# Performance work log

Measured on AMD Instinct MI355X. Metric: run time of the kernel, lower is better.

Reference implementation:

```python
import math
import jax, jax.numpy as jnp
import numpy as np

SCALE = math.sqrt(128.0)  # NOTE: original code MULTIPLIES by sqrt(128)
DROPOUT_P = 0.1


def setup_inputs() -> dict:
    key = jax.random.key(0)
    kq, kk, kv = jax.random.split(key, 3)
    B, Q, V, H = 4, 4096, 4096, 128
    return {
        "query": jax.random.normal(kq, (B, Q, H), dtype=jnp.float32),
        "key": jax.random.normal(kk, (B, V, H), dtype=jnp.float32),
        "value": jax.random.normal(kv, (B, V, H), dtype=jnp.float32),
    }


def reference(query, key, value):
    # qk: [B, Q, V]
    qk = jnp.einsum("bqh,bvh->bqv", query, key)
    scaled_qk = qk * SCALE
    softmax_qk = jax.nn.softmax(scaled_qk, axis=-1)
    # inverted dropout with a fixed RNG key (deterministic reference)
    dk = jax.random.key(42)
    keep = jax.random.bernoulli(dk, 1.0 - DROPOUT_P, softmax_qk.shape)
    dropout_qk = jnp.where(keep, softmax_qk / (1.0 - DROPOUT_P), 0.0)
    # output: [B, Q, H]
    return jnp.einsum("bqv,bvh->bqh", dropout_qk, value)
```

## Files before the change

### kernel.cpp

```cpp
#include <hip/hip_runtime.h>
#include <stdint.h>

#define NBATCH 4
#define NQ 4096
#define NV 4096
#define HD 128

#define SCL2E ((float)(11.31370849898476 * 1.4426950408889634))

#define KEEP_THRESH 3865470464u
#define EPS_SKIP 1e-6f

#define TILE_USH 24576
#define WS_NEEDED ((size_t)NBATCH * 64 * TILE_USH * 2)

#define PSTR 72
#define VLSTR 142

#define KSTR 144
#define VSTR 76

typedef __attribute__((ext_vector_type(8))) short short8;
typedef __attribute__((ext_vector_type(4))) float floatx4;
typedef unsigned int uint;
typedef unsigned short ushort;

__device__ __forceinline__ ushort bf16rne(float f) {
    uint u = __float_as_uint(f);
    u = (u + 0x7fffu + ((u >> 16) & 1u)) >> 16;
    return (ushort)u;
}
__device__ __forceinline__ float bf2f(ushort h) {
    return __uint_as_float(((uint)h) << 16);
}

template <int CTRL>
__device__ __forceinline__ float dppmov(float x) {
    return __int_as_float(__builtin_amdgcn_update_dpp(
        0, __float_as_int(x), CTRL, 0xF, 0xF, true));
}
__device__ __forceinline__ float row_max16(float x) {
    x = fmaxf(x, dppmov<0xB1>(x));
    x = fmaxf(x, dppmov<0x4E>(x));
    x = fmaxf(x, dppmov<0x141>(x));
    x = fmaxf(x, dppmov<0x140>(x));
    return x;
}
__device__ __forceinline__ float row_sum16(float x) {
    x += dppmov<0xB1>(x);
    x += dppmov<0x4E>(x);
    x += dppmov<0x141>(x);
    x += dppmov<0x140>(x);
    return x;
}

__device__ __forceinline__ uint rotl(uint x, int r) { return (x << r) | (x >> (32 - r)); }

__device__ __forceinline__ uint threefry_bits(uint j) {
    uint x0 = 0u;
    uint x1 = j;
    const uint k0 = 0u, k1 = 42u, k2 = 0u ^ 42u ^ 0x1BD11BDAu;
    x0 += k0; x1 += k1;
#define TFR4(a,b,c,d) \
    x0 += x1; x1 = rotl(x1, a); x1 ^= x0; \
    x0 += x1; x1 = rotl(x1, b); x1 ^= x0; \
    x0 += x1; x1 = rotl(x1, c); x1 ^= x0; \
    x0 += x1; x1 = rotl(x1, d); x1 ^= x0;
    TFR4(13, 15, 26, 6)
    x0 += k1; x1 += k2 + 1u;
    TFR4(17, 29, 16, 24)
    x0 += k2; x1 += k0 + 2u;
    TFR4(13, 15, 26, 6)
    x0 += k0; x1 += k1 + 3u;
    TFR4(17, 29, 16, 24)
    x0 += k1; x1 += k2 + 4u;
    TFR4(13, 15, 26, 6)
    x0 += k2; x1 += k0 + 5u;
#undef TFR4
    return x0 ^ x1;
}

__global__ __launch_bounds__(256)
void prepass(const float* __restrict__ Kg, const float* __restrict__ Vg,
             ushort* __restrict__ W) {
    __shared__ ushort vls[64 * VLSTR];
    const int rec  = blockIdx.x >> 1;
    const int half = blockIdx.x & 1;
    const int bb = rec >> 6;
    const int t  = rec & 63;
    const int v0 = t * 64;
    const size_t kvbase = (size_t)bb * NV * HD;
    ushort* dst = W + ((size_t)bb * 64 + t) * TILE_USH;
    const int tid = threadIdx.x;

    if (half == 0) {
        ushort* dkh = dst;
        ushort* dkl = dst + 8192;
#pragma unroll
        for (int i = 0; i < 4; ++i) {
            int lc = i * 256 + tid;
            int v = lc >> 4, c = lc & 15;
            const float* src = Kg + kvbase + (size_t)(v0 + v) * HD + c * 8;
            float x[8];
            *(float4*)&x[0] = *(const float4*)src;
            *(float4*)&x[4] = *(const float4*)(src + 4);
            uint H[4], L[4];
#pragma unroll
            for (int k = 0; k < 4; ++k) {
                ushort h0 = bf16rne(x[2 * k]),     h1 = bf16rne(x[2 * k + 1]);
                ushort l0 = bf16rne(x[2 * k] - bf2f(h0));
                ushort l1 = bf16rne(x[2 * k + 1] - bf2f(h1));
                H[k] = (uint)h0 | ((uint)h1 << 16);
                L[k] = (uint)l0 | ((uint)l1 << 16);
            }
            int pos = (((c >> 2) * 4 + (v >> 4)) * 64 + (c & 3) * 16 + (v & 15)) * 8;
            *(uint4*)&dkh[pos] = *(uint4*)H;
            *(uint4*)&dkl[pos] = *(uint4*)L;
        }
    } else {
        ushort* dvt = dst + 16384;
#pragma unroll
        for (int i = 0; i < 8; ++i) {
            int idx = i * 256 + tid;
            int v = idx >> 5, hq = idx & 31;
            float4 a = *(const float4*)(Vg + kvbase + (size_t)(v0 + v) * HD + hq * 4);
            uint w0 = (uint)bf16rne(a.x) | ((uint)bf16rne(a.y) << 16);
            uint w1 = (uint)bf16rne(a.z) | ((uint)bf16rne(a.w) << 16);
            *(uint*)&vls[v * VLSTR + hq * 4]     = w0;
            *(uint*)&vls[v * VLSTR + hq * 4 + 2] = w1;
        }
        __syncthreads();
#pragma unroll
        for (int i = 0; i < 4; ++i) {
            int lc = i * 256 + tid;
            int h = lc >> 3, c2 = lc & 7;
            uint Wd[4];
#pragma unroll
            for (int m = 0; m < 8; m += 2) {
                ushort a  = vls[(c2 * 8 + m) * VLSTR + h];
                ushort b2 = vls[(c2 * 8 + m + 1) * VLSTR + h];
                Wd[m >> 1] = (uint)a | ((uint)b2 << 16);
            }
            int pos = (((c2 >> 2) * 8 + (h >> 4)) * 64 + (c2 & 3) * 16 + (h & 15)) * 8;
            *(uint4*)&dvt[pos] = *(uint4*)Wd;
        }
    }
}

__global__ __launch_bounds__(256, 2)
void fa_mfma7(const float* __restrict__ Qg, const ushort* __restrict__ Wk,
              float* __restrict__ Og) {
    __shared__ ushort pls[4][32 * PSTR];
    __shared__ float obuf[3][32 * 128];
    __shared__ float mlbuf[3][32][2];

    const int tid  = threadIdx.x;
    const int wave = tid >> 6;
    const int lane = tid & 63;
    const int r    = lane & 15;
    const int qd   = lane >> 4;
    const int blockRow0 = blockIdx.x * 32;
    const int b = blockRow0 >> 12;
    const ushort* kvw = Wk + (size_t)b * 64 * TILE_USH;

    short8 qfh[2][4], qfl[2][4];
#pragma unroll
    for (int mr = 0; mr < 2; ++mr) {
        const float* qp = Qg + (size_t)(blockRow0 + mr * 16 + r) * HD + qd * 8;
#pragma unroll
        for (int kc = 0; kc < 4; ++kc) {
            float x[8];
            *(float4*)&x[0] = *(const float4*)(qp + kc * 32);
            *(float4*)&x[4] = *(const float4*)(qp + kc * 32 + 4);
#pragma unroll
            for (int j = 0; j < 8; ++j) {
                ushort h = bf16rne(x[j]);
                qfh[mr][kc][j] = (short)h;
                qfl[mr][kc][j] = (short)bf16rne(x[j] - bf2f(h));
            }
        }
    }

    floatx4 oacc[2][8];
#pragma unroll
    for (int mr = 0; mr < 2; ++mr)
#pragma unroll
        for (int n = 0; n < 8; ++n) oacc[mr][n] = (floatx4){0.f, 0.f, 0.f, 0.f};
    float m2[2][4], lr[2][4];
#pragma unroll
    for (int mr = 0; mr < 2; ++mr)
#pragma unroll
        for (int g = 0; g < 4; ++g) { m2[mr][g] = -INFINITY; lr[mr][g] = 0.f; }

    for (int t = wave; t < 64; t += 4) {
        const ushort* tK = kvw + (size_t)t * TILE_USH;
        const ushort* tV = tK + 16384;
        const int v0 = t * 64;

        floatx4 cf[2][4];
#pragma unroll
        for (int mr = 0; mr < 2; ++mr)
#pragma unroll
            for (int nb = 0; nb < 4; ++nb) cf[mr][nb] = (floatx4){0.f, 0.f, 0.f, 0.f};
#pragma unroll
        for (int kc = 0; kc < 4; ++kc) {
            short8 kh[4], kl[4];
#pragma unroll
            for (int nb = 0; nb < 4; ++nb) {
                int off = ((kc * 4 + nb) * 64 + lane) * 8;
                kh[nb] = *(const short8*)&tK[off];
                kl[nb] = *(const short8*)&tK[8192 + off];
            }
#pragma unroll
            for (int nb = 0; nb < 4; ++nb)
#pragma unroll
                for (int mr = 0; mr < 2; ++mr) {
                    cf[mr][nb] = __builtin_amdgcn_mfma_f32_16x16x32_bf16(qfh[mr][kc], kh[nb], cf[mr][nb], 0, 0, 0);
                    cf[mr][nb] = __builtin_amdgcn_mfma_f32_16x16x32_bf16(qfh[mr][kc], kl[nb], cf[mr][nb], 0, 0, 0);
                    cf[mr][nb] = __builtin_amdgcn_mfma_f32_16x16x32_bf16(qfl[mr][kc], kh[nb], cf[mr][nb], 0, 0, 0);
                }
        }

        bool act[2];
#pragma unroll
        for (int mr = 0; mr < 2; ++mr) {
            float ts[4][4], p[4][4], alpha[4], lnew[4], tsum[4];
#pragma unroll
            for (int nb = 0; nb < 4; ++nb)
#pragma unroll
                for (int g = 0; g < 4; ++g) ts[nb][g] = cf[mr][nb][g] * SCL2E;
#pragma unroll
            for (int g = 0; g < 4; ++g) {
                float tmx = fmaxf(fmaxf(ts[0][g], ts[1][g]), fmaxf(ts[2][g], ts[3][g]));
                tmx = row_max16(tmx);
                float mn = fmaxf(m2[mr][g], tmx);
                alpha[g] = __builtin_amdgcn_exp2f(m2[mr][g] - mn);
                m2[mr][g] = mn;
            }
#pragma unroll
            for (int g = 0; g < 4; ++g) {
                float s = 0.f;
#pragma unroll
                for (int nb = 0; nb < 4; ++nb) {
                    p[nb][g] = __builtin_amdgcn_exp2f(ts[nb][g] - m2[mr][g]);
                    s += p[nb][g];
                }
                s = row_sum16(s);
                tsum[g] = s;
                lnew[g] = lr[mr][g] * alpha[g] + s;
                lr[mr][g] = lnew[g];
            }
            bool rowneed = false;
#pragma unroll
            for (int g = 0; g < 4; ++g) rowneed |= (tsum[g] > EPS_SKIP * lnew[g]);
            act[mr] = __any(rowneed);

            if (act[mr]) {
#pragma unroll
                for (int n = 0; n < 8; ++n)
#pragma unroll
                    for (int g = 0; g < 4; ++g) oacc[mr][n][g] *= alpha[g];
#pragma unroll
                for (int nb = 0; nb < 4; ++nb) {
#pragma unroll
                    for (int g = 0; g < 4; ++g) {
                        if (__any(p[nb][g] > EPS_SKIP * lnew[g])) {
                            uint j = (uint)(blockRow0 + mr * 16 + qd * 4 + g) * (uint)NV
                                   + (uint)(v0 + nb * 16 + r);
                            if (threefry_bits(j) >= KEEP_THRESH) p[nb][g] = 0.f;
                        }
                        pls[wave][(mr * 16 + qd * 4 + g) * PSTR + nb * 16 + r] =
                            (ushort)(__float_as_uint(p[nb][g]) >> 16);
                    }
                }
            }
        }

        if (act[0] | act[1]) {
            __asm__ volatile("s_waitcnt lgkmcnt(0)" ::: "memory");
#pragma unroll
            for (int mr = 0; mr < 2; ++mr) {
                if (!act[mr]) continue;
#pragma unroll
                for (int kc2 = 0; kc2 < 2; ++kc2) {
                    short8 pa = *(const short8*)&pls[wave][(mr * 16 + r) * PSTR + kc2 * 32 + qd * 8];
#pragma unroll
                    for (int n = 0; n < 8; ++n) {
                        short8 vb = *(const short8*)&tV[((kc2 * 8 + n) * 64 + lane) * 8];
                        oacc[mr][n] = __builtin_amdgcn_mfma_f32_16x16x32_bf16(pa, vb, oacc[mr][n], 0, 0, 0);
                    }
                }
            }
        }
    }

    if (wave >= 1) {
#pragma unroll
        for (int mr = 0; mr < 2; ++mr) {
            if (r == 0) {
#pragma unroll
                for (int g = 0; g < 4; ++g) {
                    mlbuf[wave - 1][mr * 16 + qd * 4 + g][0] = m2[mr][g];
                    mlbuf[wave - 1][mr * 16 + qd * 4 + g][1] = lr[mr][g];
                }
            }
#pragma unroll
            for (int n = 0; n < 8; ++n)
#pragma unroll
                for (int g = 0; g < 4; ++g)
                    obuf[wave - 1][(mr * 16 + qd * 4 + g) * 128 + n * 16 + r] = oacc[mr][n][g];
        }
    }
    __syncthreads();
    if (wave == 0) {
#pragma unroll
        for (int mr = 0; mr < 2; ++mr) {
            float a0[4], aw[3][4], inv[4];
#pragma unroll
            for (int g = 0; g < 4; ++g) {
                int row = mr * 16 + qd * 4 + g;
                float mn = m2[mr][g];
#pragma unroll
                for (int i = 0; i < 3; ++i) mn = fmaxf(mn, mlbuf[i][row][0]);
                a0[g] = __builtin_amdgcn_exp2f(m2[mr][g] - mn);
                float l = lr[mr][g] * a0[g];
#pragma unroll
                for (int i = 0; i < 3; ++i) {
                    aw[i][g] = __builtin_amdgcn_exp2f(mlbuf[i][row][0] - mn);
                    l += mlbuf[i][row][1] * aw[i][g];
                }
                inv[g] = 1.0f / (0.9f * l);
            }
#pragma unroll
            for (int n = 0; n < 8; ++n)
#pragma unroll
                for (int g = 0; g < 4; ++g) {
                    int row = mr * 16 + qd * 4 + g;
                    float o = oacc[mr][n][g] * a0[g];
#pragma unroll
                    for (int i = 0; i < 3; ++i)
                        o += obuf[i][row * 128 + n * 16 + r] * aw[i][g];
                    Og[(size_t)(blockRow0 + row) * HD + n * 16 + r] = o * inv[g];
                }
        }
    }
}

__global__ __launch_bounds__(256)
void fa_mfma(const float* __restrict__ Qg, const float* __restrict__ Kg,
             const float* __restrict__ Vg, float* __restrict__ Og) {
    __shared__ ushort khi[64 * KSTR];
    __shared__ ushort klo[64 * KSTR];
    __shared__ ushort vt[128 * VSTR];
    __shared__ ushort plsf[4][16 * PSTR];

    const int tid  = threadIdx.x;
    const int wave = tid >> 6;
    const int lane = tid & 63;
    const int r    = lane & 15;
    const int qd   = lane >> 4;
    const int blockRow0 = blockIdx.x * 64;
    const int b = blockRow0 >> 12;
    const int waveRow0 = blockRow0 + wave * 16;
    const size_t kvbase = (size_t)b * NV * HD;

    short8 qfh[4], qfl[4];
    {
        const float* qp = Qg + (size_t)(waveRow0 + r) * HD + qd * 8;
#pragma unroll
        for (int kc = 0; kc < 4; ++kc) {
            float x[8];
            *(float4*)&x[0] = *(const float4*)(qp + kc * 32);
            *(float4*)&x[4] = *(const float4*)(qp + kc * 32 + 4);
#pragma unroll
            for (int j = 0; j < 8; ++j) {
                ushort h = bf16rne(x[j]);
                qfh[kc][j] = (short)h;
                qfl[kc][j] = (short)bf16rne(x[j] - bf2f(h));
            }
        }
    }

    floatx4 oacc[8];
#pragma unroll
    for (int n = 0; n < 8; ++n) oacc[n] = (floatx4){0.f, 0.f, 0.f, 0.f};
    float m2[4] = {-INFINITY, -INFINITY, -INFINITY, -INFINITY};
    float lr[4] = {0.f, 0.f, 0.f, 0.f};

    for (int v0 = 0; v0 < NV; v0 += 64) {
        __syncthreads();
#pragma unroll
        for (int i = 0; i < 8; ++i) {
            int f = i * 256 + tid;
            int v = f >> 5;
            int h = (f & 31) * 4;
            float4 kv = *(const float4*)(Kg + kvbase + (size_t)(v0 + v) * HD + h);
            ushort4 hh, ll;
            hh.x = bf16rne(kv.x); ll.x = bf16rne(kv.x - bf2f(hh.x));
            hh.y = bf16rne(kv.y); ll.y = bf16rne(kv.y - bf2f(hh.y));
            hh.z = bf16rne(kv.z); ll.z = bf16rne(kv.z - bf2f(hh.z));
            hh.w = bf16rne(kv.w); ll.w = bf16rne(kv.w - bf2f(hh.w));
            *(ushort4*)&khi[v * KSTR + h] = hh;
            *(ushort4*)&klo[v * KSTR + h] = ll;
        }
        {
            int hp = tid & 63, rp = tid >> 6;
            int h = hp * 2;
            const float* vpb = Vg + kvbase + (size_t)v0 * HD + h;
#pragma unroll
            for (int i = 0; i < 8; ++i) {
                int v = i * 8 + rp * 2;
                float2 a = *(const float2*)(vpb + (size_t)v * HD);
                float2 c = *(const float2*)(vpb + (size_t)(v + 1) * HD);
                uint w0 = (uint)bf16rne(a.x) | ((uint)bf16rne(c.x) << 16);
                uint w1 = (uint)bf16rne(a.y) | ((uint)bf16rne(c.y) << 16);
                *(uint*)&vt[h * VSTR + v]       = w0;
                *(uint*)&vt[(h + 1) * VSTR + v] = w1;
            }
        }
        __syncthreads();

        floatx4 cf[4];
#pragma unroll
        for (int nb = 0; nb < 4; ++nb) cf[nb] = (floatx4){0.f, 0.f, 0.f, 0.f};
#pragma unroll
        for (int kc = 0; kc < 4; ++kc) {
#pragma unroll
            for (int nb = 0; nb < 4; ++nb) {
                int off = (nb * 16 + r) * KSTR + kc * 32 + qd * 8;
                short8 kh = *(const short8*)&khi[off];
                short8 kl = *(const short8*)&klo[off];
                cf[nb] = __builtin_amdgcn_mfma_f32_16x16x32_bf16(qfh[kc], kh, cf[nb], 0, 0, 0);
                cf[nb] = __builtin_amdgcn_mfma_f32_16x16x32_bf16(qfh[kc], kl, cf[nb], 0, 0, 0);
                cf[nb] = __builtin_amdgcn_mfma_f32_16x16x32_bf16(qfl[kc], kh, cf[nb], 0, 0, 0);
            }
        }

        float ts[4][4], p[4][4];
#pragma unroll
        for (int nb = 0; nb < 4; ++nb)
#pragma unroll
            for (int g = 0; g < 4; ++g) ts[nb][g] = cf[nb][g] * SCL2E;

        float tsum[4], alpha[4], lnew[4];
#pragma unroll
        for (int g = 0; g < 4; ++g) {
            float tmx = fmaxf(fmaxf(ts[0][g], ts[1][g]), fmaxf(ts[2][g], ts[3][g]));
#pragma unroll
            for (int off = 1; off < 16; off <<= 1)
                tmx = fmaxf(tmx, __shfl_xor(tmx, off));
            float mn = fmaxf(m2[g], tmx);
            alpha[g] = __builtin_amdgcn_exp2f(m2[g] - mn);
            m2[g] = mn;
        }
#pragma unroll
        for (int g = 0; g < 4; ++g) {
            float s = 0.f;
#pragma unroll
            for (int nb = 0; nb < 4; ++nb) {
                p[nb][g] = __builtin_amdgcn_exp2f(ts[nb][g] - m2[g]);
                s += p[nb][g];
            }
#pragma unroll
            for (int off = 1; off < 16; off <<= 1)
                s += __shfl_xor(s, off);
            tsum[g] = s;
            lnew[g] = lr[g] * alpha[g] + s;
            lr[g] = lnew[g];
        }

        bool rowneed = false;
#pragma unroll
        for (int g = 0; g < 4; ++g) rowneed |= (tsum[g] > 1e-8f * lnew[g]);

        if (__any(rowneed)) {
#pragma unroll
            for (int n = 0; n < 8; ++n)
#pragma unroll
                for (int g = 0; g < 4; ++g) oacc[n][g] *= alpha[g];

#pragma unroll
            for (int nb = 0; nb < 4; ++nb) {
                bool nbneed = false;
#pragma unroll
                for (int g = 0; g < 4; ++g) nbneed |= (p[nb][g] > 1e-8f * lnew[g]);
                if (__any(nbneed)) {
#pragma unroll
                    for (int g = 0; g < 4; ++g) {
                        uint j = (uint)(waveRow0 + qd * 4 + g) * (uint)NV
                               + (uint)(v0 + nb * 16 + r);
                        if (threefry_bits(j) >= KEEP_THRESH) p[nb][g] = 0.f;
                    }
                }
#pragma unroll
                for (int g = 0; g < 4; ++g)
                    plsf[wave][(qd * 4 + g) * PSTR + nb * 16 + r] = bf16rne(p[nb][g]);
            }
            __asm__ volatile("s_waitcnt lgkmcnt(0)" ::: "memory");

#pragma unroll
            for (int kc2 = 0; kc2 < 2; ++kc2) {
                short8 pa = *(const short8*)&plsf[wave][r * PSTR + kc2 * 32 + qd * 8];
#pragma unroll
                for (int n = 0; n < 8; ++n) {
                    int off = (n * 16 + r) * VSTR + kc2 * 32 + qd * 8;
                    ushort4 u0 = *(const ushort4*)&vt[off];
                    ushort4 u1 = *(const ushort4*)&vt[off + 4];
                    short8 vb;
                    vb[0] = (short)u0.x; vb[1] = (short)u0.y; vb[2] = (short)u0.z; vb[3] = (short)u0.w;
                    vb[4] = (short)u1.x; vb[5] = (short)u1.y; vb[6] = (short)u1.z; vb[7] = (short)u1.w;
                    oacc[n] = __builtin_amdgcn_mfma_f32_16x16x32_bf16(pa, vb, oacc[n], 0, 0, 0);
                }
            }
        }
    }

    float inv[4];
#pragma unroll
    for (int g = 0; g < 4; ++g) inv[g] = 1.0f / (0.9f * lr[g]);
#pragma unroll
    for (int n = 0; n < 8; ++n)
#pragma unroll
        for (int g = 0; g < 4; ++g)
            Og[(size_t)(waveRow0 + qd * 4 + g) * HD + n * 16 + r] = oacc[n][g] * inv[g];
}

extern "C" void kernel_launch(void* const* d_in, const int* in_sizes, int n_in,
                              void* d_out, int out_size, void* d_ws, size_t ws_size,
                              hipStream_t stream) {
    (void)in_sizes; (void)n_in; (void)out_size;
    const float* Qg = (const float*)d_in[0];
    const float* Kg = (const float*)d_in[1];
    const float* Vg = (const float*)d_in[2];
    float* Og = (float*)d_out;
    if (ws_size >= WS_NEEDED) {
        ushort* W = (ushort*)d_ws;
        prepass<<<dim3(512), 256, 0, stream>>>(Kg, Vg, W);
        fa_mfma7<<<dim3(NBATCH * NQ / 32), 256, 0, stream>>>(Qg, (const ushort*)W, Og);
    } else {
        fa_mfma<<<dim3(NBATCH * NQ / 64), 256, 0, stream>>>(Qg, Kg, Vg, Og);
    }
}
```

Before: 199.0 us.

## Split KV tiles across eight waves with shared running max and tree merge

Doubles the block to 512 threads so eight waves each take every eighth KV tile, and merges partial softmax states with a log-depth tree reduction through shared memory. Tiles are skipped using a block-shared per-row running max with a fixed log2 margin, replacing the relative-sum epsilon test. The scale is folded into Q before the bf16 split, and the accumulator rescale is skipped when the max does not grow. The goal is more parallelism per row block and less exp, rescale and dropout-hash work on tiles that contribute nothing. The cost is more barriers and lower register budget per thread, and the margin-based skip is an approximation that differs from the old epsilon criterion.

```diff
diff --git a/kernel.cpp b/kernel.cpp
--- a/kernel.cpp
+++ b/kernel.cpp
@@ -9,7 +9,9 @@
 #define SCL2E ((float)(11.31370849898476 * 1.4426950408889634))
 
 #define KEEP_THRESH 3865470464u
-#define EPS_SKIP 1e-6f
+
+#define SKIP_MARGIN 27.0f
+#define DROP_MARGIN 20.0f
 
 #define TILE_USH 24576
 #define WS_NEEDED ((size_t)NBATCH * 64 * TILE_USH * 2)
@@ -147,12 +149,12 @@
     }
 }
 
-__global__ __launch_bounds__(256, 2)
+__global__ __launch_bounds__(512, 4)
 void fa_mfma7(const float* __restrict__ Qg, const ushort* __restrict__ Wk,
               float* __restrict__ Og) {
-    __shared__ ushort pls[4][32 * PSTR];
-    __shared__ float obuf[3][32 * 128];
-    __shared__ float mlbuf[3][32][2];
+    __shared__ __align__(16) float smemf[16384];
+    __shared__ float mlbuf[4][32][2];
+    __shared__ float gmx[32];
 
     const int tid  = threadIdx.x;
     const int wave = tid >> 6;
@@ -162,6 +164,9 @@
     const int blockRow0 = blockIdx.x * 32;
     const int b = blockRow0 >> 12;
     const ushort* kvw = Wk + (size_t)b * 64 * TILE_USH;
+    ushort* pls = (ushort*)smemf + wave * (32 * PSTR);
+
+    if (tid < 32) gmx[tid] = -1e30f;
 
     short8 qfh[2][4], qfl[2][4];
 #pragma unroll
@@ -174,9 +179,10 @@
             *(float4*)&x[4] = *(const float4*)(qp + kc * 32 + 4);
 #pragma unroll
             for (int j = 0; j < 8; ++j) {
-                ushort h = bf16rne(x[j]);
+                float xs = x[j] * SCL2E;
+                ushort h = bf16rne(xs);
                 qfh[mr][kc][j] = (short)h;
-                qfl[mr][kc][j] = (short)bf16rne(x[j] - bf2f(h));
+                qfl[mr][kc][j] = (short)bf16rne(xs - bf2f(h));
             }
         }
     }
@@ -190,9 +196,11 @@
 #pragma unroll
     for (int mr = 0; mr < 2; ++mr)
 #pragma unroll
-        for (int g = 0; g < 4; ++g) { m2[mr][g] = -INFINITY; lr[mr][g] = 0.f; }
-
-    for (int t = wave; t < 64; t += 4) {
+        for (int g = 0; g < 4; ++g) { m2[mr][g] = -1e30f; lr[mr][g] = 0.f; }
+
+    __syncthreads();
+
+    for (int t = wave; t < 64; t += 8) {
         const ushort* tK = kvw + (size_t)t * TILE_USH;
         const ushort* tV = tK + 16384;
         const int v0 = t * 64;
@@ -224,54 +232,70 @@
         bool act[2];
 #pragma unroll
         for (int mr = 0; mr < 2; ++mr) {
-            float ts[4][4], p[4][4], alpha[4], lnew[4], tsum[4];
-#pragma unroll
-            for (int nb = 0; nb < 4; ++nb)
-#pragma unroll
-                for (int g = 0; g < 4; ++g) ts[nb][g] = cf[mr][nb][g] * SCL2E;
+            float tmx[4], gm[4];
 #pragma unroll
             for (int g = 0; g < 4; ++g) {
-                float tmx = fmaxf(fmaxf(ts[0][g], ts[1][g]), fmaxf(ts[2][g], ts[3][g]));
-                tmx = row_max16(tmx);
-                float mn = fmaxf(m2[mr][g], tmx);
-                alpha[g] = __builtin_amdgcn_exp2f(m2[mr][g] - mn);
-                m2[mr][g] = mn;
-            }
+                float v = fmaxf(fmaxf(cf[mr][0][g], cf[mr][1][g]),
+                                fmaxf(cf[mr][2][g], cf[mr][3][g]));
+                tmx[g] = row_max16(v);
+            }
+            bool rowact = false;
+#pragma unroll
+            for (int g = 0; g < 4; ++g) {
+                gm[g] = gmx[mr * 16 + qd * 4 + g];
+                rowact |= (tmx[g] > fmaxf(m2[mr][g], gm[g]) - SKIP_MARGIN);
+            }
+#pragma unroll
+            for (int g = 0; g < 4; ++g)
+                if (r == 0 && tmx[g] > gm[g]) gmx[mr * 16 + qd * 4 + g] = tmx[g];
+            act[mr] = __any(rowact);
+            if (!act[mr]) continue;
+
+            float alpha[4];
+            bool nm = false;
+#pragma unroll
+            for (int g = 0; g < 4; ++g) nm |= (tmx[g] > m2[mr][g]);
+            if (__any(nm)) {
+#pragma unroll
+                for (int g = 0; g < 4; ++g) {
+                    float mn = fmaxf(m2[mr][g], tmx[g]);
+                    alpha[g] = __builtin_amdgcn_exp2f(m2[mr][g] - mn);
+                    m2[mr][g] = mn;
+                }
+#pragma unroll
+                for (int n = 0; n < 8; ++n)
+#pragma unroll
+                    for (int g = 0; g < 4; ++g) oacc[mr][n][g] *= alpha[g];
+            } else {
+#pragma unroll
+                for (int g = 0; g < 4; ++g) alpha[g] = 1.f;
+            }
+
+            float p[4][4], thr[4];
 #pragma unroll
             for (int g = 0; g < 4; ++g) {
                 float s = 0.f;
 #pragma unroll
                 for (int nb = 0; nb < 4; ++nb) {
-                    p[nb][g] = __builtin_amdgcn_exp2f(ts[nb][g] - m2[mr][g]);
+                    p[nb][g] = __builtin_amdgcn_exp2f(cf[mr][nb][g] - m2[mr][g]);
                     s += p[nb][g];
                 }
                 s = row_sum16(s);
-                tsum[g] = s;
-                lnew[g] = lr[mr][g] * alpha[g] + s;
-                lr[mr][g] = lnew[g];
-            }
-            bool rowneed = false;
-#pragma unroll
-            for (int g = 0; g < 4; ++g) rowneed |= (tsum[g] > EPS_SKIP * lnew[g]);
-            act[mr] = __any(rowneed);
-
-            if (act[mr]) {
-#pragma unroll
-                for (int n = 0; n < 8; ++n)
-#pragma unroll
-                    for (int g = 0; g < 4; ++g) oacc[mr][n][g] *= alpha[g];
-#pragma unroll
-                for (int nb = 0; nb < 4; ++nb) {
-#pragma unroll
-                    for (int g = 0; g < 4; ++g) {
-                        if (__any(p[nb][g] > EPS_SKIP * lnew[g])) {
-                            uint j = (uint)(blockRow0 + mr * 16 + qd * 4 + g) * (uint)NV
-                                   + (uint)(v0 + nb * 16 + r);
-                            if (threefry_bits(j) >= KEEP_THRESH) p[nb][g] = 0.f;
-                        }
-                        pls[wave][(mr * 16 + qd * 4 + g) * PSTR + nb * 16 + r] =
-                            (ushort)(__float_as_uint(p[nb][g]) >> 16);
+                lr[mr][g] = lr[mr][g] * alpha[g] + s;
+                thr[g] = fmaxf(gm[g], m2[mr][g]) - DROP_MARGIN;
+            }
+
+#pragma unroll
+            for (int nb = 0; nb < 4; ++nb) {
+#pragma unroll
+                for (int g = 0; g < 4; ++g) {
+                    if (__any(cf[mr][nb][g] > thr[g])) {
+                        uint j = (uint)(blockRow0 + mr * 16 + qd * 4 + g) * (uint)NV
+                               + (uint)(v0 + nb * 16 + r);
+                        if (threefry_bits(j) >= KEEP_THRESH) p[nb][g] = 0.f;
                     }
+                    pls[(mr * 16 + qd * 4 + g) * PSTR + nb * 16 + r] =
+                        (ushort)(__float_as_uint(p[nb][g]) >> 16);
                 }
             }
         }
@@ -283,7 +307,7 @@
                 if (!act[mr]) continue;
 #pragma unroll
                 for (int kc2 = 0; kc2 < 2; ++kc2) {
-                    short8 pa = *(const short8*)&pls[wave][(mr * 16 + r) * PSTR + kc2 * 32 + qd * 8];
+                    short8 pa = *(const short8*)&pls[(mr * 16 + r) * PSTR + kc2 * 32 + qd * 8];
 #pragma unroll
                     for (int n = 0; n < 8; ++n) {
                         short8 vb = *(const short8*)&tV[((kc2 * 8 + n) * 64 + lane) * 8];
@@ -294,54 +318,67 @@
         }
     }
 
-    if (wave >= 1) {
+    auto publish = [&](int buf) {
 #pragma unroll
         for (int mr = 0; mr < 2; ++mr) {
             if (r == 0) {
 #pragma unroll
                 for (int g = 0; g < 4; ++g) {
-                    mlbuf[wave - 1][mr * 16 + qd * 4 + g][0] = m2[mr][g];
-                    mlbuf[wave - 1][mr * 16 + qd * 4 + g][1] = lr[mr][g];
+                    mlbuf[buf][mr * 16 + qd * 4 + g][0] = m2[mr][g];
+                    mlbuf[buf][mr * 16 + qd * 4 + g][1] = lr[mr][g];
                 }
             }
 #pragma unroll
             for (int n = 0; n < 8; ++n)
 #pragma unroll
                 for (int g = 0; g < 4; ++g)
-                    obuf[wave - 1][(mr * 16 + qd * 4 + g) * 128 + n * 16 + r] = oacc[mr][n][g];
-        }
-    }
-    __syncthreads();
-    if (wave == 0) {
-#pragma unroll
-        for (int mr = 0; mr < 2; ++mr) {
-            float a0[4], aw[3][4], inv[4];
+                    smemf[buf * 4096 + (mr * 16 + qd * 4 + g) * 128 + n * 16 + r] =
+                        oacc[mr][n][g];
+        }
+    };
+    auto absorb = [&](int buf) {
+#pragma unroll
+        for (int mr = 0; mr < 2; ++mr)
 #pragma unroll
             for (int g = 0; g < 4; ++g) {
                 int row = mr * 16 + qd * 4 + g;
-                float mn = m2[mr][g];
-#pragma unroll
-                for (int i = 0; i < 3; ++i) mn = fmaxf(mn, mlbuf[i][row][0]);
-                a0[g] = __builtin_amdgcn_exp2f(m2[mr][g] - mn);
-                float l = lr[mr][g] * a0[g];
-#pragma unroll
-                for (int i = 0; i < 3; ++i) {
-                    aw[i][g] = __builtin_amdgcn_exp2f(mlbuf[i][row][0] - mn);
-                    l += mlbuf[i][row][1] * aw[i][g];
-                }
-                inv[g] = 1.0f / (0.9f * l);
-            }
+                float mb = mlbuf[buf][row][0], lb = mlbuf[buf][row][1];
+                float mn = fmaxf(m2[mr][g], mb);
+                float aa = __builtin_amdgcn_exp2f(m2[mr][g] - mn);
+                float ab = __builtin_amdgcn_exp2f(mb - mn);
+                lr[mr][g] = lr[mr][g] * aa + lb * ab;
+                m2[mr][g] = mn;
+#pragma unroll
+                for (int n = 0; n < 8; ++n)
+                    oacc[mr][n][g] = oacc[mr][n][g] * aa
+                                   + smemf[buf * 4096 + row * 128 + n * 16 + r] * ab;
+            }
+    };
+
+    __syncthreads();
+    if (wave & 1) publish(wave >> 1);
+    __syncthreads();
+    if (!(wave & 1)) absorb(wave >> 1);
+    __syncthreads();
+    if (wave == 2 || wave == 6) publish(wave >> 2);
+    __syncthreads();
+    if (wave == 0 || wave == 4) absorb(wave >> 2);
+    __syncthreads();
+    if (wave == 4) publish(0);
+    __syncthreads();
+    if (wave == 0) {
+        absorb(0);
+#pragma unroll
+        for (int mr = 0; mr < 2; ++mr) {
+            float inv[4];
+#pragma unroll
+            for (int g = 0; g < 4; ++g) inv[g] = 1.0f / (0.9f * lr[mr][g]);
 #pragma unroll
             for (int n = 0; n < 8; ++n)
 #pragma unroll
-                for (int g = 0; g < 4; ++g) {
-                    int row = mr * 16 + qd * 4 + g;
-                    float o = oacc[mr][n][g] * a0[g];
-#pragma unroll
-                    for (int i = 0; i < 3; ++i)
-                        o += obuf[i][row * 128 + n * 16 + r] * aw[i][g];
-                    Og[(size_t)(blockRow0 + row) * HD + n * 16 + r] = o * inv[g];
-                }
+                for (int g = 0; g < 4; ++g)
+                    Og[(size_t)(blockRow0 + mr * 16 + qd * 4 + g) * HD + n * 16 + r] =
+                        oacc[mr][n][g] * inv[g];
         }
     }
 }
@@ -536,7 +573,7 @@
     if (ws_size >= WS_NEEDED) {
         ushort* W = (ushort*)d_ws;
         prepass<<<dim3(512), 256, 0, stream>>>(Kg, Vg, W);
-        fa_mfma7<<<dim3(NBATCH * NQ / 32), 256, 0, stream>>>(Qg, (const ushort*)W, Og);
+        fa_mfma7<<<dim3(NBATCH * NQ / 32), 512, 0, stream>>>(Qg, (const ushort*)W, Og);
     } else {
         fa_mfma<<<dim3(NBATCH * NQ / 64), 256, 0, stream>>>(Qg, Kg, Vg, Og);
     }
```

Result: slower. 447.6 us (+124.9%).
